# Optimization experiments

Hardware: AMD Instinct MI355X
Metric: run time of the kernel (lower is better)

The kernel has to match this reference:

```python
import jax, jax.numpy as jnp
import numpy as np

B, S, H = 8, 2048, 768      # batch, seq_len, hidden_size
N = 512                     # spans per example
MAXW = 30                   # max span width (length in [0, MAXW-1] -> width <= MAXW)


def setup_inputs() -> dict:
    key = jax.random.key(0)
    k1, k2, k3, k4 = jax.random.split(key, 4)
    embeddings = jax.random.normal(k1, (B, S, H), dtype=jnp.float32)
    starts = jax.random.randint(k2, (B, N), 0, S - MAXW)          # span starts
    lengths = jax.random.randint(k3, (B, N), 0, MAXW)             # end = start + length
    w = jax.random.normal(k4, (H, 1), dtype=jnp.float32) * 0.02   # nn.Linear(hidden, 1) weight (transposed)
    b = jnp.zeros((1,), dtype=jnp.float32)                        # linear bias
    return {"embeddings": embeddings, "w": w, "b": b, "starts": starts, "lengths": lengths}


def reference(embeddings, w, b, starts, lengths):
    # Vectorized ragged span pooling: gather up to MAXW tokens per span,
    # masked softmax over attention scores, then concat [start, end, attn].
    ends = starts + lengths                                  # inclusive end index
    offs = jnp.arange(MAXW)                                  # (W,)
    positions = starts[..., None] + offs                     # (B, N, W)
    mask = offs[None, None, :] <= lengths[..., None]         # (B, N, W) valid-token mask

    gather = jax.vmap(lambda e, p: e[p])                     # per-example gather
    span_emb = gather(embeddings, positions)                 # (B, N, W, H)

    scores = span_emb @ w + b                                # (B, N, W, 1)
    scores = jnp.where(mask[..., None], scores, -jnp.inf)
    attn_w = jax.nn.softmax(scores, axis=2)                  # masked softmax over span width
    attn_out = jnp.sum(attn_w * span_emb, axis=2)            # (B, N, H)

    start_emb = gather(embeddings, starts)                   # (B, N, H)
    end_emb = gather(embeddings, ends)                       # (B, N, H)
    return jnp.concatenate([start_emb, end_emb, attn_out], axis=-1)  # (B, N, 3H)
```

## Files before the change

kernel.cpp:

```cpp
#include <hip/hip_runtime.h>
#include <hip/hip_bf16.h>
#include <math.h>

#define BB 8
#define SS 2048
#define HH 768
#define NN 512
#define MAXW 30

__global__ __launch_bounds__(256) void sort_spans_kernel(
    const int* __restrict__ starts,
    int*       __restrict__ order)
{
    const int b   = blockIdx.x;
    const int tid = threadIdx.x;
    __shared__ int hist[SS];
    __shared__ int partial[256];

    for (int i = tid; i < SS; i += 256) hist[i] = 0;
    __syncthreads();

    const int* st = starts + b * NN;
    for (int n = tid; n < NN; n += 256) atomicAdd(&hist[st[n]], 1);
    __syncthreads();

    const int base = tid * 8;
    int s = 0;
    #pragma unroll
    for (int k = 0; k < 8; ++k) s += hist[base + k];
    partial[tid] = s;
    __syncthreads();

    if (tid == 0) {
        int acc = 0;
        for (int i = 0; i < 256; ++i) { int v = partial[i]; partial[i] = acc; acc += v; }
    }
    __syncthreads();

    int acc = partial[tid];
    #pragma unroll
    for (int k = 0; k < 8; ++k) { int v = hist[base + k]; hist[base + k] = acc; acc += v; }
    __syncthreads();

    for (int n = tid; n < NN; n += 256) {
        int pos = atomicAdd(&hist[st[n]], 1);
        order[b * NN + pos] = n;
    }
}

__global__ __launch_bounds__(256) void span_repr_kernel(
    const float* __restrict__ emb,
    const float* __restrict__ w,
    const float* __restrict__ bias,
    const int*   __restrict__ starts,
    const int*   __restrict__ lengths,
    const int*   __restrict__ order,
    float*       __restrict__ out)
{
    const int bi = blockIdx.x & 7;
    const int r  = blockIdx.x >> 3;
    const int n  = order ? order[bi * NN + r] : r;
    const int span = bi * NN + n;
    const int tid  = threadIdx.x;

    const int start = starts[span];
    const int len   = lengths[span];

    const float* ebase = emb + (size_t)bi * SS * HH;

    __shared__ float s_w[HH];
    __shared__ float s_scores[MAXW];
    __shared__ float s_p[MAXW];

    #pragma unroll
    for (int k = 0; k < 3; ++k) s_w[tid + k * 256] = w[tid + k * 256];
    __syncthreads();

    {
        const int g  = tid >> 3;
        const int lg = tid & 7;
        if (g <= len) {
            const float* row = ebase + (size_t)(start + g) * HH;
            float acc = 0.f;
            #pragma unroll
            for (int j = 0; j < 24; ++j) {
                const int h = (lg + j * 8) * 4;
                float4 e4 = *reinterpret_cast<const float4*>(row + h);
                float4 w4 = *reinterpret_cast<const float4*>(s_w + h);
                acc += e4.x * w4.x + e4.y * w4.y + e4.z * w4.z + e4.w * w4.w;
            }
            acc += __shfl_xor(acc, 1);
            acc += __shfl_xor(acc, 2);
            acc += __shfl_xor(acc, 4);
            if (lg == 0) s_scores[g] = acc + bias[0];
        }
    }
    __syncthreads();

    if (tid < 64) {
        const bool valid = (tid <= len) && (tid < MAXW);
        float s = valid ? s_scores[tid] : -INFINITY;
        float m = s;
        #pragma unroll
        for (int off = 32; off; off >>= 1) m = fmaxf(m, __shfl_xor(m, off));
        float e = valid ? __expf(s - m) : 0.f;
        float sum = e;
        #pragma unroll
        for (int off = 32; off; off >>= 1) sum += __shfl_xor(sum, off);
        if (tid < MAXW) s_p[tid] = e / sum;
    }
    __syncthreads();

    if (tid < HH / 4) {
        const int h = tid * 4;
        float* orow = out + (size_t)span * (3 * HH);

        float4 acc = make_float4(0.f, 0.f, 0.f, 0.f);
        for (int t = 0; t <= len; ++t) {
            float4 e4 = *reinterpret_cast<const float4*>(
                ebase + (size_t)(start + t) * HH + h);
            if (t == 0)   *reinterpret_cast<float4*>(orow + h)      = e4;
            if (t == len) *reinterpret_cast<float4*>(orow + HH + h) = e4;
            const float p = s_p[t];
            acc.x += p * e4.x;
            acc.y += p * e4.y;
            acc.z += p * e4.z;
            acc.w += p * e4.w;
        }
        *reinterpret_cast<float4*>(orow + 2 * HH + h) = acc;
    }
}

extern "C" void kernel_launch(void* const* d_in, const int* in_sizes, int n_in,
                              void* d_out, int out_size, void* d_ws, size_t ws_size,
                              hipStream_t stream) {
    const float* emb     = (const float*)d_in[0];
    const float* w       = (const float*)d_in[1];
    const float* bias    = (const float*)d_in[2];
    const int*   starts  = (const int*)d_in[3];
    const int*   lengths = (const int*)d_in[4];
    float*       out     = (float*)d_out;

    int* order = nullptr;
    if (ws_size >= (size_t)(BB * NN * sizeof(int))) {
        order = (int*)d_ws;
        sort_spans_kernel<<<dim3(BB), dim3(256), 0, stream>>>(starts, order);
    }

    span_repr_kernel<<<dim3(BB * NN), dim3(256), 0, stream>>>(
        emb, w, bias, starts, lengths, order, out);
}
```

Baseline: 35.23 us.

## Precompute per-token scores with a dense GEMV and process one span per wavefront

```diff
diff --git a/kernel.cpp b/kernel.cpp
--- a/kernel.cpp
+++ b/kernel.cpp
@@ -8,127 +8,146 @@
 #define NN 512
 #define MAXW 30
 
-__global__ __launch_bounds__(256) void sort_spans_kernel(
-    const int* __restrict__ starts,
-    int*       __restrict__ order)
+#define GEMV_BLOCKS (BB * SS / 4)
+
+__global__ __launch_bounds__(256) void prep_kernel(
+    const float* __restrict__ emb,
+    const float* __restrict__ w,
+    const float* __restrict__ bias,
+    const int*   __restrict__ starts,
+    float*       __restrict__ scores,
+    int*         __restrict__ order,
+    int gemv_blocks)
 {
-    const int b   = blockIdx.x;
     const int tid = threadIdx.x;
-    __shared__ int hist[SS];
-    __shared__ int partial[256];
-
-    for (int i = tid; i < SS; i += 256) hist[i] = 0;
-    __syncthreads();
-
-    const int* st = starts + b * NN;
-    for (int n = tid; n < NN; n += 256) atomicAdd(&hist[st[n]], 1);
-    __syncthreads();
-
-    const int base = tid * 8;
-    int s = 0;
-    #pragma unroll
-    for (int k = 0; k < 8; ++k) s += hist[base + k];
-    partial[tid] = s;
-    __syncthreads();
-
-    if (tid == 0) {
-        int acc = 0;
-        for (int i = 0; i < 256; ++i) { int v = partial[i]; partial[i] = acc; acc += v; }
-    }
-    __syncthreads();
-
-    int acc = partial[tid];
-    #pragma unroll
-    for (int k = 0; k < 8; ++k) { int v = hist[base + k]; hist[base + k] = acc; acc += v; }
-    __syncthreads();
-
-    for (int n = tid; n < NN; n += 256) {
-        int pos = atomicAdd(&hist[st[n]], 1);
-        order[b * NN + pos] = n;
+    if ((int)blockIdx.x < gemv_blocks) {
+        const int wv = tid >> 6, lane = tid & 63;
+        const int token = blockIdx.x * 4 + wv;
+        const float* row = emb + (size_t)token * HH;
+        const int h0 = lane * 4;
+        float acc = 0.f;
+        #pragma unroll
+        for (int k = 0; k < 3; ++k) {
+            float4 e4 = *reinterpret_cast<const float4*>(row + h0 + k * 256);
+            float4 w4 = *reinterpret_cast<const float4*>(w + h0 + k * 256);
+            acc += e4.x * w4.x + e4.y * w4.y + e4.z * w4.z + e4.w * w4.w;
+        }
+        #pragma unroll
+        for (int off = 32; off; off >>= 1) acc += __shfl_xor(acc, off);
+        if (lane == 0) scores[token] = acc + bias[0];
+    } else {
+        const int b = blockIdx.x - gemv_blocks;
+        __shared__ int hist[SS];
+        __shared__ int partial[256];
+        for (int i = tid; i < SS; i += 256) hist[i] = 0;
+        __syncthreads();
+        const int* st = starts + b * NN;
+        for (int n = tid; n < NN; n += 256) atomicAdd(&hist[st[n]], 1);
+        __syncthreads();
+        const int base = tid * 8;
+        int s = 0;
+        #pragma unroll
+        for (int k = 0; k < 8; ++k) s += hist[base + k];
+        partial[tid] = s;
+        __syncthreads();
+        if (tid == 0) {
+            int a = 0;
+            for (int i = 0; i < 256; ++i) { int v = partial[i]; partial[i] = a; a += v; }
+        }
+        __syncthreads();
+        int a = partial[tid];
+        #pragma unroll
+        for (int k = 0; k < 8; ++k) { int v = hist[base + k]; hist[base + k] = a; a += v; }
+        __syncthreads();
+        for (int n = tid; n < NN; n += 256) {
+            int pos = atomicAdd(&hist[st[n]], 1);
+            order[b * NN + pos] = n;
+        }
     }
 }
 
-__global__ __launch_bounds__(256) void span_repr_kernel(
+__global__ __launch_bounds__(256) void span_kernel(
     const float* __restrict__ emb,
     const float* __restrict__ w,
     const float* __restrict__ bias,
     const int*   __restrict__ starts,
     const int*   __restrict__ lengths,
     const int*   __restrict__ order,
+    const float* __restrict__ scores,
     float*       __restrict__ out)
 {
-    const int bi = blockIdx.x & 7;
-    const int r  = blockIdx.x >> 3;
-    const int n  = order ? order[bi * NN + r] : r;
+    const int tid  = threadIdx.x;
+    const int wv   = tid >> 6;
+    const int lane = tid & 63;
+    const int bi   = blockIdx.x & 7;
+    const int rank = ((int)blockIdx.x >> 3) * 4 + wv;
+    const int n    = order ? order[bi * NN + rank] : rank;
     const int span = bi * NN + n;
-    const int tid  = threadIdx.x;
 
     const int start = starts[span];
     const int len   = lengths[span];
 
-    const float* ebase = emb + (size_t)bi * SS * HH;
+    const float* ebase = emb + (size_t)bi * SS * HH + (size_t)start * HH;
+    const int h0 = lane * 4;
 
-    __shared__ float s_w[HH];
-    __shared__ float s_scores[MAXW];
-    __shared__ float s_p[MAXW];
-
-    #pragma unroll
-    for (int k = 0; k < 3; ++k) s_w[tid + k * 256] = w[tid + k * 256];
-    __syncthreads();
-
-    {
-        const int g  = tid >> 3;
-        const int lg = tid & 7;
-        if (g <= len) {
-            const float* row = ebase + (size_t)(start + g) * HH;
-            float acc = 0.f;
+    float sc;
+    if (scores) {
+        sc = (lane <= len) ? scores[bi * SS + start + lane] : -INFINITY;
+    } else {
+        float4 w0 = *reinterpret_cast<const float4*>(w + h0);
+        float4 w1 = *reinterpret_cast<const float4*>(w + h0 + 256);
+        float4 w2 = *reinterpret_cast<const float4*>(w + h0 + 512);
+        sc = -INFINITY;
+        for (int t = 0; t <= len; ++t) {
+            const float* row = ebase + (size_t)t * HH;
+            float4 v0 = *reinterpret_cast<const float4*>(row + h0);
+            float4 v1 = *reinterpret_cast<const float4*>(row + h0 + 256);
+            float4 v2 = *reinterpret_cast<const float4*>(row + h0 + 512);
+            float d = v0.x * w0.x + v0.y * w0.y + v0.z * w0.z + v0.w * w0.w
+                    + v1.x * w1.x + v1.y * w1.y + v1.z * w1.z + v1.w * w1.w
+                    + v2.x * w2.x + v2.y * w2.y + v2.z * w2.z + v2.w * w2.w;
             #pragma unroll
-            for (int j = 0; j < 24; ++j) {
-                const int h = (lg + j * 8) * 4;
-                float4 e4 = *reinterpret_cast<const float4*>(row + h);
-                float4 w4 = *reinterpret_cast<const float4*>(s_w + h);
-                acc += e4.x * w4.x + e4.y * w4.y + e4.z * w4.z + e4.w * w4.w;
-            }
-            acc += __shfl_xor(acc, 1);
-            acc += __shfl_xor(acc, 2);
-            acc += __shfl_xor(acc, 4);
-            if (lg == 0) s_scores[g] = acc + bias[0];
+            for (int off = 32; off; off >>= 1) d += __shfl_xor(d, off);
+            if (lane == t) sc = d + bias[0];
         }
     }
-    __syncthreads();
 
-    if (tid < 64) {
-        const bool valid = (tid <= len) && (tid < MAXW);
-        float s = valid ? s_scores[tid] : -INFINITY;
-        float m = s;
-        #pragma unroll
-        for (int off = 32; off; off >>= 1) m = fmaxf(m, __shfl_xor(m, off));
-        float e = valid ? __expf(s - m) : 0.f;
-        float sum = e;
-        #pragma unroll
-        for (int off = 32; off; off >>= 1) sum += __shfl_xor(sum, off);
-        if (tid < MAXW) s_p[tid] = e / sum;
+    float m = sc;
+    #pragma unroll
+    for (int off = 32; off; off >>= 1) m = fmaxf(m, __shfl_xor(m, off));
+    float e = (lane <= len) ? __expf(sc - m) : 0.f;
+    float sum = e;
+    #pragma unroll
+    for (int off = 32; off; off >>= 1) sum += __shfl_xor(sum, off);
+    const float p = e / sum;
+
+    float* orow = out + (size_t)span * (3 * HH);
+    float4 a0 = make_float4(0.f, 0.f, 0.f, 0.f);
+    float4 a1 = a0, a2 = a0;
+    const float* row = ebase;
+    for (int t = 0; t <= len; ++t) {
+        const float pt = __shfl(p, t);
+        float4 v0 = *reinterpret_cast<const float4*>(row + h0);
+        float4 v1 = *reinterpret_cast<const float4*>(row + h0 + 256);
+        float4 v2 = *reinterpret_cast<const float4*>(row + h0 + 512);
+        if (t == 0) {
+            *reinterpret_cast<float4*>(orow + h0)       = v0;
+            *reinterpret_cast<float4*>(orow + h0 + 256) = v1;
+            *reinterpret_cast<float4*>(orow + h0 + 512) = v2;
+        }
+        if (t == len) {
+            *reinterpret_cast<float4*>(orow + HH + h0)       = v0;
+            *reinterpret_cast<float4*>(orow + HH + h0 + 256) = v1;
+            *reinterpret_cast<float4*>(orow + HH + h0 + 512) = v2;
+        }
+        a0.x += pt * v0.x; a0.y += pt * v0.y; a0.z += pt * v0.z; a0.w += pt * v0.w;
+        a1.x += pt * v1.x; a1.y += pt * v1.y; a1.z += pt * v1.z; a1.w += pt * v1.w;
+        a2.x += pt * v2.x; a2.y += pt * v2.y; a2.z += pt * v2.z; a2.w += pt * v2.w;
+        row += HH;
     }
-    __syncthreads();
-
-    if (tid < HH / 4) {
-        const int h = tid * 4;
-        float* orow = out + (size_t)span * (3 * HH);
-
-        float4 acc = make_float4(0.f, 0.f, 0.f, 0.f);
-        for (int t = 0; t <= len; ++t) {
-            float4 e4 = *reinterpret_cast<const float4*>(
-                ebase + (size_t)(start + t) * HH + h);
-            if (t == 0)   *reinterpret_cast<float4*>(orow + h)      = e4;
-            if (t == len) *reinterpret_cast<float4*>(orow + HH + h) = e4;
-            const float p = s_p[t];
-            acc.x += p * e4.x;
-            acc.y += p * e4.y;
-            acc.z += p * e4.z;
-            acc.w += p * e4.w;
-        }
-        *reinterpret_cast<float4*>(orow + 2 * HH + h) = acc;
-    }
+    *reinterpret_cast<float4*>(orow + 2 * HH + h0)       = a0;
+    *reinterpret_cast<float4*>(orow + 2 * HH + h0 + 256) = a1;
+    *reinterpret_cast<float4*>(orow + 2 * HH + h0 + 512) = a2;
 }
 
 extern "C" void kernel_launch(void* const* d_in, const int* in_sizes, int n_in,
@@ -141,12 +160,24 @@
     const int*   lengths = (const int*)d_in[4];
     float*       out     = (float*)d_out;
 
-    int* order = nullptr;
-    if (ws_size >= (size_t)(BB * NN * sizeof(int))) {
+    const size_t scores_bytes = (size_t)BB * SS * sizeof(float);
+    const size_t order_bytes  = (size_t)BB * NN * sizeof(int);
+
+    float* scores = nullptr;
+    int*   order  = nullptr;
+    if (ws_size >= scores_bytes + order_bytes) {
+        scores = (float*)d_ws;
+        order  = (int*)((char*)d_ws + scores_bytes);
+    } else if (ws_size >= order_bytes) {
         order = (int*)d_ws;
-        sort_spans_kernel<<<dim3(BB), dim3(256), 0, stream>>>(starts, order);
     }
 
-    span_repr_kernel<<<dim3(BB * NN), dim3(256), 0, stream>>>(
-        emb, w, bias, starts, lengths, order, out);
+    if (scores || order) {
+        const int gemv_blocks = scores ? GEMV_BLOCKS : 0;
+        prep_kernel<<<dim3(gemv_blocks + BB), dim3(256), 0, stream>>>(
+            emb, w, bias, starts, scores, order, gemv_blocks);
+    }
+
+    span_kernel<<<dim3(BB * NN / 4), dim3(256), 0, stream>>>(
+        emb, w, bias, starts, lengths, order, scores, out);
 }
```

Result: slower. 37.60 us (+6.7%).
